# Optimization experiments

Measured on AMD Instinct MI355X. Metric: run time of the kernel, lower is better.

The kernel has to match this reference:

```python
import jax, jax.numpy as jnp
import numpy as np

B, TE, TD, HE, HD = 8, 256, 256, 512, 512


def setup_inputs() -> dict:
    key = jax.random.key(0)
    k1, k2, k3, k4, k5 = jax.random.split(key, 5)
    return {
        "encoder_out_seq": jax.random.normal(k1, (B, TE, HE), dtype=jnp.float32),
        "decoder_out_seq": jax.random.normal(k2, (B, TD, HD), dtype=jnp.float32),
        "W_a": jax.random.normal(k3, (HE, HE), dtype=jnp.float32) * 0.05,
        "U_a": jax.random.normal(k4, (HD, HE), dtype=jnp.float32) * 0.05,
        "V_a": jax.random.normal(k5, (HE, 1), dtype=jnp.float32) * 0.05,
    }


def reference(encoder_out_seq, decoder_out_seq, W_a, U_a, V_a):
    # Bahdanau additive attention, vectorized over all decoder timesteps.
    # Hoist encoder projection (the K.rnn version recomputed this each step).
    Ws = jnp.einsum('bth,hk->btk', encoder_out_seq, W_a)      # [B, Te, He]
    Uh = jnp.einsum('bdh,hk->bdk', decoder_out_seq, U_a)     # [B, Td, He]
    # tanh(S.Wa + hj.Ua) -> score via V_a, softmax over encoder axis Te
    scores = jnp.einsum('bdtk,k->bdt',
                        jnp.tanh(Ws[:, None, :, :] + Uh[:, :, None, :]),
                        V_a[:, 0])                            # [B, Td, Te]
    e = jax.nn.softmax(scores, axis=-1)                       # energies
    c = jnp.einsum('bdt,bth->bdh', e, encoder_out_seq)        # contexts [B, Td, He]
    return c, e
```

## Files before the change

kernel.cpp:

```cpp
#include <hip/hip_runtime.h>


#define BB  8
#define TEE 256
#define TDD 256
#define HH  512
#define C2LOG2E 2.8853900817779268f

typedef __attribute__((ext_vector_type(8))) short  short8;
typedef __attribute__((ext_vector_type(4))) float  floatx4;

__device__ __forceinline__ unsigned short f2bf(float f) {
  unsigned int u = __builtin_bit_cast(unsigned int, f);
  u += 0x7FFFu + ((u >> 16) & 1u);
  return (unsigned short)(u >> 16);
}

__global__ __launch_bounds__(256) void prep_kernel(
    const float* __restrict__ Wa, const float* __restrict__ Ua,
    const float* __restrict__ enc,
    unsigned short* __restrict__ WTa, unsigned short* __restrict__ WTu,
    unsigned short* __restrict__ encT)
{
  __shared__ float tile[64][65];
  const int c = threadIdx.x & 63, r4 = threadIdx.x >> 6;
  const int z = blockIdx.z;

  if (z < 2) {
    const float* W = z ? Ua : Wa;
    unsigned short* WT = z ? WTu : WTa;
    const int k0 = blockIdx.x * 64, n0 = blockIdx.y * 64;
    #pragma unroll
    for (int i = 0; i < 16; ++i) {
      int kr = i * 4 + r4;
      tile[kr][c] = W[(size_t)(k0 + kr) * HH + n0 + c];
    }
    __syncthreads();
    #pragma unroll
    for (int i = 0; i < 16; ++i) {
      int nr = i * 4 + r4;
      WT[(size_t)(n0 + nr) * HH + k0 + c] = f2bf(tile[c][nr] * C2LOG2E);
    }
  } else {
    if (blockIdx.y >= 4) return;
    const int b = z - 2;
    const int h0 = blockIdx.x * 64, t0 = blockIdx.y * 64;
    #pragma unroll
    for (int i = 0; i < 16; ++i) {
      int tr = i * 4 + r4;
      tile[tr][c] = enc[((size_t)b * TEE + t0 + tr) * HH + h0 + c];
    }
    __syncthreads();
    #pragma unroll
    for (int i = 0; i < 16; ++i) {
      int hr = i * 4 + r4;
      encT[((size_t)b * HH + h0 + hr) * TEE + t0 + c] = f2bf(tile[c][hr]);
    }
  }
}

__global__ __launch_bounds__(256) void proj_exp(
    const float* __restrict__ enc, const float* __restrict__ dec,
    const unsigned short* __restrict__ WTa, const unsigned short* __restrict__ WTu,
    float* __restrict__ EW, float* __restrict__ EU)
{
  const float* X = blockIdx.z ? dec : enc;
  const unsigned short* WT = blockIdx.z ? WTu : WTa;
  float* Y = blockIdx.z ? EU : EW;
  const int lane = threadIdx.x & 63, w = threadIdx.x >> 6;
  const int m0 = blockIdx.x * 64 + w * 16, n0 = blockIdx.y * 64;
  const int r15 = lane & 15, g = lane >> 4;

  floatx4 acc[4] = {{0.f,0.f,0.f,0.f},{0.f,0.f,0.f,0.f},
                    {0.f,0.f,0.f,0.f},{0.f,0.f,0.f,0.f}};
  const float* ap = X + (size_t)(m0 + r15) * HH + g * 8;
  const unsigned short* bp0 = WT + (size_t)(n0 + r15) * HH + g * 8;

  for (int k0 = 0; k0 < HH; k0 += 32) {
    float4 a0 = *(const float4*)(ap + k0);
    float4 a1 = *(const float4*)(ap + k0 + 4);
    short8 a;
    a[0]=(short)f2bf(a0.x); a[1]=(short)f2bf(a0.y);
    a[2]=(short)f2bf(a0.z); a[3]=(short)f2bf(a0.w);
    a[4]=(short)f2bf(a1.x); a[5]=(short)f2bf(a1.y);
    a[6]=(short)f2bf(a1.z); a[7]=(short)f2bf(a1.w);
    #pragma unroll
    for (int nt = 0; nt < 4; ++nt) {
      short8 bv = *(const short8*)(bp0 + (size_t)nt * 16 * HH + k0);
      acc[nt] = __builtin_amdgcn_mfma_f32_16x16x32_bf16(a, bv, acc[nt], 0, 0, 0);
    }
  }
  #pragma unroll
  for (int nt = 0; nt < 4; ++nt) {
    float* yp = Y + (size_t)(m0 + g * 4) * HH + n0 + nt * 16 + r15;
    #pragma unroll
    for (int r = 0; r < 4; ++r) {
      float v = fminf(fmaxf(acc[nt][r], -126.f), 126.f);
      yp[(size_t)r * HH] = __builtin_amdgcn_exp2f(v);
    }
  }
}

__global__ __launch_bounds__(256) void score_db(
    const float* __restrict__ EW, const float* __restrict__ EU,
    const float* __restrict__ Va, float* __restrict__ A)
{
  __shared__ float sw[2][16][132];
  __shared__ float su[2][16][132];

  const int b  = blockIdx.z;
  const int t0 = blockIdx.x * 16, d0 = blockIdx.y * 16;
  const int tid = threadIdx.x;
  const int t = tid & 15, d = tid >> 4;
  const int srow = tid >> 4, scol = (tid & 15) * 8;

  const float* wrow = EW + (size_t)(b * TEE + t0 + srow) * HH + scol;
  const float* urow = EU + (size_t)(b * TDD + d0 + srow) * HH + scol;

  float ac0 = 0.f, ac1 = 0.f, ac2 = 0.f, ac3 = 0.f;
  float ac4 = 0.f, ac5 = 0.f, ac6 = 0.f, ac7 = 0.f;

  {
    float4 w0 = *(const float4*)(wrow);
    float4 w1 = *(const float4*)(wrow + 4);
    float4 u0 = *(const float4*)(urow);
    float4 u1 = *(const float4*)(urow + 4);
    *(float4*)&sw[0][srow][scol]     = w0;
    *(float4*)&sw[0][srow][scol + 4] = w1;
    *(float4*)&su[0][srow][scol]     = u0;
    *(float4*)&su[0][srow][scol + 4] = u1;
  }

  for (int ch = 0; ch < 4; ++ch) {
    float4 nw0, nw1, nu0, nu1;
    const bool more = (ch + 1) < 4;
    if (more) {
      const int kn = (ch + 1) * 128;
      nw0 = *(const float4*)(wrow + kn);
      nw1 = *(const float4*)(wrow + kn + 4);
      nu0 = *(const float4*)(urow + kn);
      nu1 = *(const float4*)(urow + kn + 4);
    }
    __syncthreads();

    const float (*swc)[132] = sw[ch & 1];
    const float (*suc)[132] = su[ch & 1];
    const float* vbase = Va + ch * 128;

#define TERM(W_, U_, V_, AC_) { \
    float z_ = fmaf((W_), (U_), 1.0f);           \
    float r_ = __builtin_amdgcn_rcpf(z_);        \
    AC_ = fmaf((V_), r_, AC_); }

    #pragma unroll 4
    for (int kk = 0; kk < 128; kk += 8) {
      float4 wA = *(const float4*)&swc[t][kk];
      float4 wB = *(const float4*)&swc[t][kk + 4];
      float4 uA = *(const float4*)&suc[d][kk];
      float4 uB = *(const float4*)&suc[d][kk + 4];
      float4 vA = *(const float4*)(vbase + kk);
      float4 vB = *(const float4*)(vbase + kk + 4);
      TERM(wA.x, uA.x, vA.x, ac0) TERM(wA.y, uA.y, vA.y, ac1)
      TERM(wA.z, uA.z, vA.z, ac2) TERM(wA.w, uA.w, vA.w, ac3)
      TERM(wB.x, uB.x, vB.x, ac4) TERM(wB.y, uB.y, vB.y, ac5)
      TERM(wB.z, uB.z, vB.z, ac6) TERM(wB.w, uB.w, vB.w, ac7)
    }
#undef TERM

    if (more) {
      const int nb = (ch + 1) & 1;
      *(float4*)&sw[nb][srow][scol]     = nw0;
      *(float4*)&sw[nb][srow][scol + 4] = nw1;
      *(float4*)&su[nb][srow][scol]     = nu0;
      *(float4*)&su[nb][srow][scol + 4] = nu1;
    }
  }
  float s = ((ac0 + ac1) + (ac2 + ac3)) + ((ac4 + ac5) + (ac6 + ac7));
  A[(size_t)(b * TDD + d0 + d) * TEE + t0 + t] = s;
}

__global__ __launch_bounds__(256) void ctx_fused(
    const float* __restrict__ A, const unsigned short* __restrict__ encT,
    float* __restrict__ c, float* __restrict__ e_out)
{
  __shared__ unsigned short pe[16][264];

  const int b  = blockIdx.z;
  const int d0 = blockIdx.x * 16;
  const int h0 = blockIdx.y * 256;
  const int lane = threadIdx.x & 63, w = threadIdx.x >> 6;

  {
    const int row  = w * 4 + (lane >> 4);
    const int col0 = (lane & 15) * 16;
    const float* ar = A + ((size_t)(b * TDD + d0 + row)) * TEE + col0;
    float x[16];
    #pragma unroll
    for (int j = 0; j < 4; ++j) {
      float4 v = *(const float4*)(ar + j * 4);
      x[4*j] = v.x; x[4*j+1] = v.y; x[4*j+2] = v.z; x[4*j+3] = v.w;
    }
    float m = x[0];
    #pragma unroll
    for (int j = 1; j < 16; ++j) m = fminf(m, x[j]);
    #pragma unroll
    for (int off = 8; off; off >>= 1) m = fminf(m, __shfl_xor(m, off));
    float p[16], s = 0.f;
    #pragma unroll
    for (int j = 0; j < 16; ++j) {
      p[j] = __builtin_amdgcn_exp2f(C2LOG2E * (m - x[j]));
      s += p[j];
    }
    #pragma unroll
    for (int off = 8; off; off >>= 1) s += __shfl_xor(s, off);
    float r = __builtin_amdgcn_rcpf(s);

    float* er = e_out + ((size_t)(b * TDD + d0 + row)) * TEE + col0;
    #pragma unroll
    for (int j = 0; j < 16; ++j) {
      float v = p[j] * r;
      pe[row][col0 + j] = f2bf(v);
      if (blockIdx.y == 0) er[j] = v;
    }
  }
  __syncthreads();

  const int r15 = lane & 15, g = lane >> 4;
  const int hw = h0 + w * 64;
  floatx4 acc[4] = {{0.f,0.f,0.f,0.f},{0.f,0.f,0.f,0.f},
                    {0.f,0.f,0.f,0.f},{0.f,0.f,0.f,0.f}};
  const unsigned short* bp0 = encT + ((size_t)b * HH + hw + r15) * TEE + g * 8;

  for (int k0 = 0; k0 < TEE; k0 += 32) {
    short8 a = *(const short8*)(&pe[r15][k0 + g * 8]);
    #pragma unroll
    for (int nt = 0; nt < 4; ++nt) {
      short8 bv = *(const short8*)(bp0 + (size_t)nt * 16 * TEE + k0);
      acc[nt] = __builtin_amdgcn_mfma_f32_16x16x32_bf16(a, bv, acc[nt], 0, 0, 0);
    }
  }
  #pragma unroll
  for (int nt = 0; nt < 4; ++nt) {
    float* cp = c + (size_t)(b * TDD + d0 + g * 4) * HH + hw + nt * 16 + r15;
    #pragma unroll
    for (int r = 0; r < 4; ++r) cp[(size_t)r * HH] = acc[nt][r];
  }
}

extern "C" void kernel_launch(void* const* d_in, const int* in_sizes, int n_in,
                              void* d_out, int out_size, void* d_ws, size_t ws_size,
                              hipStream_t stream) {
  const float* enc = (const float*)d_in[0];
  const float* dec = (const float*)d_in[1];
  const float* Wa  = (const float*)d_in[2];
  const float* Ua  = (const float*)d_in[3];
  const float* Va  = (const float*)d_in[4];

  float* c_out = (float*)d_out;
  float* e_out = c_out + (size_t)BB * TDD * HH;

  unsigned short* WTa  = (unsigned short*)d_ws;
  unsigned short* WTu  = WTa + (size_t)HH * HH;
  unsigned short* encT = WTu + (size_t)HH * HH;
  float* EW  = (float*)(encT + (size_t)BB * HH * TEE);
  float* EU  = EW + (size_t)BB * TEE * HH;
  float* Asc = EU + (size_t)BB * TDD * HH;

  prep_kernel<<<dim3(8, 8, 10),  256, 0, stream>>>(Wa, Ua, enc, WTa, WTu, encT);
  proj_exp   <<<dim3(32, 8, 2),  256, 0, stream>>>(enc, dec, WTa, WTu, EW, EU);
  score_db   <<<dim3(16, 16, 8), 256, 0, stream>>>(EW, EU, Va, Asc);
  ctx_fused  <<<dim3(16, 2, 8),  256, 0, stream>>>(Asc, encT, c_out, e_out);
}
```

Before: 75.25 us.

## Register-tile score kernel with split-K partials reduced in softmax kernel

The score kernel changes from one output per thread over 16x16 tiles to a 4x4 register tile per thread over 64x64 tiles. K is split into four slabs whose partial sums go to separate buffers, and shared memory holds transposed operands so each k step loads vectors. The context kernel now sums the four partial slabs before the softmax and handles 32 decoder rows per block. This cuts shared-memory traffic per rcp/fma term in the tanh-score loop, which is the dominant cost. In exchange it adds extra partial-score global traffic, and the double-buffered prefetch is dropped.

```diff
diff --git a/kernel.cpp b/kernel.cpp
--- a/kernel.cpp
+++ b/kernel.cpp
@@ -6,6 +6,7 @@
 #define TDD 256
 #define HH  512
 #define C2LOG2E 2.8853900817779268f
+#define SLAB ((size_t)BB * TDD * TEE)
 
 typedef __attribute__((ext_vector_type(8))) short  short8;
 typedef __attribute__((ext_vector_type(4))) float  floatx4;
@@ -101,138 +102,142 @@
   }
 }
 
-__global__ __launch_bounds__(256) void score_db(
+__global__ __launch_bounds__(256) void score_rt(
     const float* __restrict__ EW, const float* __restrict__ EU,
-    const float* __restrict__ Va, float* __restrict__ A)
-{
-  __shared__ float sw[2][16][132];
-  __shared__ float su[2][16][132];
+    const float* __restrict__ Va, float* __restrict__ Apart)
+{
+  __shared__ float swT[32][68];
+  __shared__ float suT[32][68];
 
   const int b  = blockIdx.z;
-  const int t0 = blockIdx.x * 16, d0 = blockIdx.y * 16;
+  const int ks = blockIdx.x >> 2;
+  const int t0 = (blockIdx.x & 3) * 64;
+  const int d0 = blockIdx.y * 64;
+  const int kbase = ks * 128;
   const int tid = threadIdx.x;
-  const int t = tid & 15, d = tid >> 4;
-  const int srow = tid >> 4, scol = (tid & 15) * 8;
-
-  const float* wrow = EW + (size_t)(b * TEE + t0 + srow) * HH + scol;
-  const float* urow = EU + (size_t)(b * TDD + d0 + srow) * HH + scol;
-
-  float ac0 = 0.f, ac1 = 0.f, ac2 = 0.f, ac3 = 0.f;
-  float ac4 = 0.f, ac5 = 0.f, ac6 = 0.f, ac7 = 0.f;
+  const int tx = tid & 15, ty = tid >> 4;
+  const int sr = tid >> 2, fq = tid & 3;
+
+  const float* wsrc = EW + ((size_t)(b * TEE) + t0 + sr) * HH + kbase;
+  const float* usrc = EU + ((size_t)(b * TDD) + d0 + sr) * HH + kbase;
+
+  float acc[4][4] = {};
+
+  for (int ch = 0; ch < 4; ++ch) {
+    const int kc = ch * 32;
+    float4 w0 = *(const float4*)(wsrc + kc + fq * 4);
+    float4 w1 = *(const float4*)(wsrc + kc + fq * 4 + 16);
+    float4 u0 = *(const float4*)(usrc + kc + fq * 4);
+    float4 u1 = *(const float4*)(usrc + kc + fq * 4 + 16);
+    __syncthreads();
+    {
+      const int kq = fq * 4;
+      swT[kq + 0][sr] = w0.x; swT[kq + 1][sr] = w0.y;
+      swT[kq + 2][sr] = w0.z; swT[kq + 3][sr] = w0.w;
+      swT[kq + 16][sr] = w1.x; swT[kq + 17][sr] = w1.y;
+      swT[kq + 18][sr] = w1.z; swT[kq + 19][sr] = w1.w;
+      suT[kq + 0][sr] = u0.x; suT[kq + 1][sr] = u0.y;
+      suT[kq + 2][sr] = u0.z; suT[kq + 3][sr] = u0.w;
+      suT[kq + 16][sr] = u1.x; suT[kq + 17][sr] = u1.y;
+      suT[kq + 18][sr] = u1.z; suT[kq + 19][sr] = u1.w;
+    }
+    __syncthreads();
+
+    const float* vb = Va + kbase + kc;
+#define T1(WI_, UJ_, AJI_) { \
+    float z_ = fmaf((WI_), (UJ_), 1.0f); \
+    AJI_ = fmaf(v, __builtin_amdgcn_rcpf(z_), AJI_); }
+
+    #pragma unroll 8
+    for (int k = 0; k < 32; ++k) {
+      floatx4 w = *(const floatx4*)&swT[k][tx * 4];
+      floatx4 u = *(const floatx4*)&suT[k][ty * 4];
+      float v = vb[k];
+      #pragma unroll
+      for (int j = 0; j < 4; ++j) {
+        float uj = u[j];
+        T1(w[0], uj, acc[j][0]) T1(w[1], uj, acc[j][1])
+        T1(w[2], uj, acc[j][2]) T1(w[3], uj, acc[j][3])
+      }
+    }
+#undef T1
+  }
+
+  float* Ap = Apart + (size_t)ks * SLAB;
+  #pragma unroll
+  for (int j = 0; j < 4; ++j) {
+    const int d = d0 + ty * 4 + j;
+    floatx4 o = {acc[j][0], acc[j][1], acc[j][2], acc[j][3]};
+    *(floatx4*)(Ap + ((size_t)(b * TDD) + d) * TEE + t0 + tx * 4) = o;
+  }
+}
+
+__global__ __launch_bounds__(256) void ctx_fused(
+    const float* __restrict__ Apart, const unsigned short* __restrict__ encT,
+    float* __restrict__ c, float* __restrict__ e_out)
+{
+  __shared__ unsigned short pe[32][264];
+
+  const int b  = blockIdx.z;
+  const int d0 = blockIdx.x * 32;
+  const int h0 = blockIdx.y * 128;
+  const int lane = threadIdx.x & 63, w = threadIdx.x >> 6;
 
   {
-    float4 w0 = *(const float4*)(wrow);
-    float4 w1 = *(const float4*)(wrow + 4);
-    float4 u0 = *(const float4*)(urow);
-    float4 u1 = *(const float4*)(urow + 4);
-    *(float4*)&sw[0][srow][scol]     = w0;
-    *(float4*)&sw[0][srow][scol + 4] = w1;
-    *(float4*)&su[0][srow][scol]     = u0;
-    *(float4*)&su[0][srow][scol + 4] = u1;
-  }
-
-  for (int ch = 0; ch < 4; ++ch) {
-    float4 nw0, nw1, nu0, nu1;
-    const bool more = (ch + 1) < 4;
-    if (more) {
-      const int kn = (ch + 1) * 128;
-      nw0 = *(const float4*)(wrow + kn);
-      nw1 = *(const float4*)(wrow + kn + 4);
-      nu0 = *(const float4*)(urow + kn);
-      nu1 = *(const float4*)(urow + kn + 4);
-    }
-    __syncthreads();
-
-    const float (*swc)[132] = sw[ch & 1];
-    const float (*suc)[132] = su[ch & 1];
-    const float* vbase = Va + ch * 128;
-
-#define TERM(W_, U_, V_, AC_) { \
-    float z_ = fmaf((W_), (U_), 1.0f);           \
-    float r_ = __builtin_amdgcn_rcpf(z_);        \
-    AC_ = fmaf((V_), r_, AC_); }
-
-    #pragma unroll 4
-    for (int kk = 0; kk < 128; kk += 8) {
-      float4 wA = *(const float4*)&swc[t][kk];
-      float4 wB = *(const float4*)&swc[t][kk + 4];
-      float4 uA = *(const float4*)&suc[d][kk];
-      float4 uB = *(const float4*)&suc[d][kk + 4];
-      float4 vA = *(const float4*)(vbase + kk);
-      float4 vB = *(const float4*)(vbase + kk + 4);
-      TERM(wA.x, uA.x, vA.x, ac0) TERM(wA.y, uA.y, vA.y, ac1)
-      TERM(wA.z, uA.z, vA.z, ac2) TERM(wA.w, uA.w, vA.w, ac3)
-      TERM(wB.x, uB.x, vB.x, ac4) TERM(wB.y, uB.y, vB.y, ac5)
-      TERM(wB.z, uB.z, vB.z, ac6) TERM(wB.w, uB.w, vB.w, ac7)
-    }
-#undef TERM
-
-    if (more) {
-      const int nb = (ch + 1) & 1;
-      *(float4*)&sw[nb][srow][scol]     = nw0;
-      *(float4*)&sw[nb][srow][scol + 4] = nw1;
-      *(float4*)&su[nb][srow][scol]     = nu0;
-      *(float4*)&su[nb][srow][scol + 4] = nu1;
-    }
-  }
-  float s = ((ac0 + ac1) + (ac2 + ac3)) + ((ac4 + ac5) + (ac6 + ac7));
-  A[(size_t)(b * TDD + d0 + d) * TEE + t0 + t] = s;
-}
-
-__global__ __launch_bounds__(256) void ctx_fused(
-    const float* __restrict__ A, const unsigned short* __restrict__ encT,
-    float* __restrict__ c, float* __restrict__ e_out)
-{
-  __shared__ unsigned short pe[16][264];
-
-  const int b  = blockIdx.z;
-  const int d0 = blockIdx.x * 16;
-  const int h0 = blockIdx.y * 256;
-  const int lane = threadIdx.x & 63, w = threadIdx.x >> 6;
-
-  {
-    const int row  = w * 4 + (lane >> 4);
-    const int col0 = (lane & 15) * 16;
-    const float* ar = A + ((size_t)(b * TDD + d0 + row)) * TEE + col0;
-    float x[16];
-    #pragma unroll
-    for (int j = 0; j < 4; ++j) {
-      float4 v = *(const float4*)(ar + j * 4);
-      x[4*j] = v.x; x[4*j+1] = v.y; x[4*j+2] = v.z; x[4*j+3] = v.w;
+    const int row  = w * 8 + (lane >> 3);
+    const int col0 = (lane & 7) * 32;
+    const size_t base = ((size_t)(b * TDD) + d0 + row) * TEE + col0;
+    float x[32];
+    #pragma unroll
+    for (int q = 0; q < 8; ++q) {
+      floatx4 v = *(const floatx4*)(Apart + base + q * 4);
+      x[4*q] = v[0]; x[4*q+1] = v[1]; x[4*q+2] = v[2]; x[4*q+3] = v[3];
+    }
+    #pragma unroll
+    for (int s = 1; s < 4; ++s) {
+      #pragma unroll
+      for (int q = 0; q < 8; ++q) {
+        floatx4 v = *(const floatx4*)(Apart + (size_t)s * SLAB + base + q * 4);
+        x[4*q] += v[0]; x[4*q+1] += v[1]; x[4*q+2] += v[2]; x[4*q+3] += v[3];
+      }
     }
     float m = x[0];
     #pragma unroll
-    for (int j = 1; j < 16; ++j) m = fminf(m, x[j]);
-    #pragma unroll
-    for (int off = 8; off; off >>= 1) m = fminf(m, __shfl_xor(m, off));
-    float p[16], s = 0.f;
-    #pragma unroll
-    for (int j = 0; j < 16; ++j) {
+    for (int j = 1; j < 32; ++j) m = fminf(m, x[j]);
+    #pragma unroll
+    for (int off = 4; off; off >>= 1) m = fminf(m, __shfl_xor(m, off));
+    float p[32], s = 0.f;
+    #pragma unroll
+    for (int j = 0; j < 32; ++j) {
       p[j] = __builtin_amdgcn_exp2f(C2LOG2E * (m - x[j]));
       s += p[j];
     }
     #pragma unroll
-    for (int off = 8; off; off >>= 1) s += __shfl_xor(s, off);
+    for (int off = 4; off; off >>= 1) s += __shfl_xor(s, off);
     float r = __builtin_amdgcn_rcpf(s);
 
-    float* er = e_out + ((size_t)(b * TDD + d0 + row)) * TEE + col0;
-    #pragma unroll
-    for (int j = 0; j < 16; ++j) {
-      float v = p[j] * r;
-      pe[row][col0 + j] = f2bf(v);
-      if (blockIdx.y == 0) er[j] = v;
+    #pragma unroll
+    for (int j = 0; j < 32; j += 2) {
+      float v0 = p[j] * r, v1 = p[j+1] * r;
+      *(ushort2*)&pe[row][col0 + j] = make_ushort2(f2bf(v0), f2bf(v1));
+    }
+    if (blockIdx.y == 0) {
+      float* er = e_out + ((size_t)(b * TDD) + d0 + row) * TEE + col0;
+      #pragma unroll
+      for (int j = 0; j < 32; ++j) er[j] = p[j] * r;
     }
   }
   __syncthreads();
 
   const int r15 = lane & 15, g = lane >> 4;
-  const int hw = h0 + w * 64;
+  const int dsub = (w & 1) * 16;
+  const int hw = h0 + (w >> 1) * 64;
   floatx4 acc[4] = {{0.f,0.f,0.f,0.f},{0.f,0.f,0.f,0.f},
                     {0.f,0.f,0.f,0.f},{0.f,0.f,0.f,0.f}};
   const unsigned short* bp0 = encT + ((size_t)b * HH + hw + r15) * TEE + g * 8;
 
   for (int k0 = 0; k0 < TEE; k0 += 32) {
-    short8 a = *(const short8*)(&pe[r15][k0 + g * 8]);
+    short8 a = *(const short8*)(&pe[dsub + r15][k0 + g * 8]);
     #pragma unroll
     for (int nt = 0; nt < 4; ++nt) {
       short8 bv = *(const short8*)(bp0 + (size_t)nt * 16 * TEE + k0);
@@ -241,7 +246,7 @@
   }
   #pragma unroll
   for (int nt = 0; nt < 4; ++nt) {
-    float* cp = c + (size_t)(b * TDD + d0 + g * 4) * HH + hw + nt * 16 + r15;
+    float* cp = c + ((size_t)(b * TDD) + d0 + dsub + g * 4) * HH + hw + nt * 16 + r15;
     #pragma unroll
     for (int r = 0; r < 4; ++r) cp[(size_t)r * HH] = acc[nt][r];
   }
@@ -262,12 +267,12 @@
   unsigned short* WTa  = (unsigned short*)d_ws;
   unsigned short* WTu  = WTa + (size_t)HH * HH;
   unsigned short* encT = WTu + (size_t)HH * HH;
-  float* EW  = (float*)(encT + (size_t)BB * HH * TEE);
-  float* EU  = EW + (size_t)BB * TEE * HH;
-  float* Asc = EU + (size_t)BB * TDD * HH;
+  float* EW    = (float*)(encT + (size_t)BB * HH * TEE);
+  float* EU    = EW + (size_t)BB * TEE * HH;
+  float* Apart = EU + (size_t)BB * TDD * HH;
 
   prep_kernel<<<dim3(8, 8, 10),  256, 0, stream>>>(Wa, Ua, enc, WTa, WTu, encT);
   proj_exp   <<<dim3(32, 8, 2),  256, 0, stream>>>(enc, dec, WTa, WTu, EW, EU);
-  score_db   <<<dim3(16, 16, 8), 256, 0, stream>>>(EW, EU, Va, Asc);
-  ctx_fused  <<<dim3(16, 2, 8),  256, 0, stream>>>(Asc, encT, c_out, e_out);
-}
+  score_rt   <<<dim3(16, 4, 8),  256, 0, stream>>>(EW, EU, Va, Apart);
+  ctx_fused  <<<dim3(8, 4, 8),   256, 0, stream>>>(Apart, encT, c_out, e_out);
+}
```

Result: slower. 79.10 us (+5.1%).
